# Optimization experiments

Hardware: AMD Instinct MI355X
Metric: run time of the kernel (lower is better)

## Reference

```python
import jax, jax.numpy as jnp
import numpy as np
import math

D_MODEL = 1024
HEADS = 16
HEAD_DIM = D_MODEL // HEADS
BATCH = 2
SEQ = 2048


def setup_inputs() -> dict:
    key = jax.random.key(0)
    ks = jax.random.split(key, 6)
    scale = 1.0 / math.sqrt(D_MODEL)
    return {
        "x": jax.random.normal(ks[0], (BATCH, SEQ, D_MODEL), dtype=jnp.float32),
        "mask": jnp.zeros((SEQ, SEQ), dtype=jnp.float32),
        "w_qkv": jax.random.normal(ks[1], (D_MODEL, 3 * D_MODEL), dtype=jnp.float32) * scale,
        "b_qkv": jax.random.normal(ks[2], (3 * D_MODEL,), dtype=jnp.float32) * 0.01,
        "w_out": jax.random.normal(ks[3], (D_MODEL, D_MODEL), dtype=jnp.float32) * scale,
        "b_out": jax.random.normal(ks[4], (D_MODEL,), dtype=jnp.float32) * 0.01,
    }


def reference(x, mask, w_qkv, b_qkv, w_out, b_out):
    B, S, D = x.shape
    H, hd = HEADS, HEAD_DIM
    # fused QKV projection: [B,S,3D]
    qkv = x @ w_qkv + b_qkv
    # [B,S,H,3*hd] -> [B,H,S,3*hd]
    qkv = qkv.reshape(B, S, H, 3 * hd).transpose(0, 2, 1, 3)
    q, k, v = jnp.split(qkv, 3, axis=-1)  # each [B,H,S,hd]
    inv_sqrt_d = jnp.asarray(1.0 / math.sqrt(hd), dtype=x.dtype)
    scores = jnp.einsum("bhqd,bhkd->bhqk", q, k) * inv_sqrt_d
    # additive mask; [S,S] broadcasts identically in [H,B,S,S] or [B,H,S,S] layout
    scores = scores + mask
    attn = jax.nn.softmax(scores, axis=-1)
    vals = jnp.einsum("bhqk,bhkd->bhqd", attn, v)  # [B,H,S,hd]
    vals = vals.transpose(0, 2, 1, 3).reshape(B, S, H * hd)
    return vals @ w_out + b_out
```

## Files before the change

### kernel.cpp

```cpp
#include <hip/hip_runtime.h>


typedef __bf16 bf16;
typedef __bf16 bf16x2 __attribute__((ext_vector_type(2)));
typedef __bf16 bf16x4 __attribute__((ext_vector_type(4)));
typedef __bf16 bf16x8 __attribute__((ext_vector_type(8)));
typedef float f32x4 __attribute__((ext_vector_type(4)));

#define MFMA(a, b, c) __builtin_amdgcn_mfma_f32_16x16x32_bf16((a), (b), (c), 0, 0, 0)

#if __has_builtin(__builtin_amdgcn_exp2f)
#define EXP2(x) __builtin_amdgcn_exp2f(x)
#else
#define EXP2(x) exp2f(x)
#endif

__device__ __forceinline__ void load_lds16(const bf16* g, void* l) {
    __builtin_amdgcn_global_load_lds(
        (const __attribute__((address_space(1))) unsigned int*)g,
        (__attribute__((address_space(3))) unsigned int*)l, 16, 0, 0);
}

__global__ void cast4_kernel(const float* __restrict__ in, bf16* __restrict__ out, int n4) {
    int i = blockIdx.x * blockDim.x + threadIdx.x;
    if (i < n4) {
        float4 v = ((const float4*)in)[i];
        bf16x4 o = {(bf16)v.x, (bf16)v.y, (bf16)v.z, (bf16)v.w};
        ((bf16x4*)out)[i] = o;
    }
}

__global__ void transpose_cast_kernel(const float* __restrict__ in, bf16* __restrict__ out,
                                      int R, int C) {
    __shared__ float tile[32][33];
    int bx = blockIdx.x * 32;
    int by = blockIdx.y * 32;
    int tx = threadIdx.x, ty = threadIdx.y;
    for (int i = 0; i < 32; i += 8)
        tile[ty + i][tx] = in[(size_t)(by + ty + i) * C + bx + tx];
    __syncthreads();
    for (int i = 0; i < 32; i += 8)
        out[(size_t)(bx + ty + i) * R + by + tx] = (bf16)tile[tx][ty + i];
}

__global__ __launch_bounds__(256) void gemm_qkv_kernel(
    const bf16* __restrict__ A, const bf16* __restrict__ BT,
    const float* __restrict__ bias,
    bf16* __restrict__ Q, bf16* __restrict__ K, bf16* __restrict__ VT) {
    __shared__ __attribute__((aligned(16))) char lds[2][16384];
    int bm = blockIdx.x, bn = blockIdx.y;
    int t = threadIdx.x;
    int w = t >> 6, lane = t & 63, g = lane >> 4, l16 = lane & 15;
    int wm = (w >> 1) * 64, wn = (w & 1) * 64;
    f32x4 acc[4][4] = {};
    const bf16* Ablk = A + (size_t)(bm * 128) * 1024;
    const bf16* Bblk = BT + (size_t)(bn * 128) * 1024;
    int srow = t >> 2;
    int scg = (t & 3) ^ (srow & 3);
    const bf16* ag0 = Ablk + (size_t)srow * 1024 + scg * 8;
    const bf16* ag1 = ag0 + 64 * 1024;
    const bf16* bg0 = Bblk + (size_t)srow * 1024 + scg * 8;
    const bf16* bg1 = bg0 + 64 * 1024;

    load_lds16(ag0, lds[0] + t * 16);
    load_lds16(ag1, lds[0] + 4096 + t * 16);
    load_lds16(bg0, lds[0] + 8192 + t * 16);
    load_lds16(bg1, lds[0] + 12288 + t * 16);
    asm volatile("s_waitcnt vmcnt(0)" ::: "memory");

    int sw = l16 & 3;
#pragma unroll 2
    for (int j = 0; j < 32; j++) {
        asm volatile("s_barrier" ::: "memory");
        int jp = j + 1 < 32 ? j + 1 : 31;
        char* dst = lds[(j + 1) & 1];
        load_lds16(ag0 + jp * 32, dst + t * 16);
        load_lds16(ag1 + jp * 32, dst + 4096 + t * 16);
        load_lds16(bg0 + jp * 32, dst + 8192 + t * 16);
        load_lds16(bg1 + jp * 32, dst + 12288 + t * 16);

        const bf16* As = (const bf16*)lds[j & 1];
        const bf16* Bs = (const bf16*)(lds[j & 1] + 8192);
        bf16x8 af[4], bfr[4];
#pragma unroll
        for (int mi = 0; mi < 4; mi++) {
            int row = wm + mi * 16 + l16;
            af[mi] = *(const bf16x8*)(&As[row * 32 + (g ^ sw) * 8]);
        }
#pragma unroll
        for (int ni = 0; ni < 4; ni++) {
            int row = wn + ni * 16 + l16;
            bfr[ni] = *(const bf16x8*)(&Bs[row * 32 + (g ^ sw) * 8]);
        }
#pragma unroll
        for (int mi = 0; mi < 4; mi++)
#pragma unroll
            for (int ni = 0; ni < 4; ni++)
                acc[mi][ni] = MFMA(bfr[ni], af[mi], acc[mi][ni]);
        asm volatile("s_waitcnt vmcnt(0)" ::: "memory");
    }
    __syncthreads();

    bf16* vt = (bf16*)lds;
    int b = bm >> 4;
    int row0 = (bm & 15) * 128 + wm;
    int half_col = bn * 128 + wn;
    int h = half_col / 192, tt = half_col % 192;
    size_t bh = (size_t)(b * 16 + h);

    if (tt < 128) {
        bf16* base = (tt == 0 ? Q : K) + bh * 2048 * 64;
#pragma unroll
        for (int mi = 0; mi < 4; mi++) {
#pragma unroll
            for (int ni = 0; ni < 4; ni++) {
                int d0 = ni * 16 + g * 4;
                float4 bv = *(const float4*)(&bias[half_col + d0]);
                int s = row0 + mi * 16 + l16;
                bf16x4 pk = {(bf16)(acc[mi][ni][0] + bv.x), (bf16)(acc[mi][ni][1] + bv.y),
                             (bf16)(acc[mi][ni][2] + bv.z), (bf16)(acc[mi][ni][3] + bv.w)};
                *(bf16x4*)(&base[(size_t)s * 64 + d0]) = pk;
            }
        }
    } else {
#pragma unroll
        for (int mi = 0; mi < 4; mi++) {
            int s_local = wm + mi * 16 + l16;
#pragma unroll
            for (int ni = 0; ni < 4; ni++) {
                int d0 = ni * 16 + g * 4;
                float4 bv = *(const float4*)(&bias[half_col + d0]);
                vt[(d0 + 0) * 136 + s_local] = (bf16)(acc[mi][ni][0] + bv.x);
                vt[(d0 + 1) * 136 + s_local] = (bf16)(acc[mi][ni][1] + bv.y);
                vt[(d0 + 2) * 136 + s_local] = (bf16)(acc[mi][ni][2] + bv.z);
                vt[(d0 + 3) * 136 + s_local] = (bf16)(acc[mi][ni][3] + bv.w);
            }
        }
    }
    __syncthreads();

    int hc0 = bn * 128, hc1 = bn * 128 + 64;
    int vhalf = (hc0 % 192 == 128) ? 0 : ((hc1 % 192 == 128) ? 1 : -1);
    if (vhalf >= 0) {
        int vcol = bn * 128 + vhalf * 64;
        size_t vbh = (size_t)(b * 16 + vcol / 192);
        int d = t >> 2, ch = t & 3;
        const bf16* src = &vt[d * 136 + ch * 32];
        bf16* dstp = &VT[(vbh * 64 + d) * 2048 + (bm & 15) * 128 + ch * 32];
#pragma unroll
        for (int k = 0; k < 4; k++)
            *(bf16x8*)(&dstp[k * 8]) = *(const bf16x8*)(&src[k * 8]);
    }
}

__global__ __launch_bounds__(256) void gemm_out_kernel(
    const bf16* __restrict__ A, const bf16* __restrict__ BT,
    const float* __restrict__ bias, float* __restrict__ out) {
    __shared__ __attribute__((aligned(16))) char lds[2][12288];
    int bm = blockIdx.x, bn = blockIdx.y;
    int t = threadIdx.x;
    int w = t >> 6, lane = t & 63, g = lane >> 4, l16 = lane & 15;
    int wm = (w >> 1) * 64, wn = (w & 1) * 32;
    f32x4 acc[4][2] = {};
    const bf16* Ablk = A + (size_t)(bm * 128) * 1024;
    const bf16* Bblk = BT + (size_t)(bn * 64) * 1024;
    int srow = t >> 2;
    int scg = (t & 3) ^ (srow & 3);
    const bf16* ag0 = Ablk + (size_t)srow * 1024 + scg * 8;
    const bf16* ag1 = ag0 + 64 * 1024;
    const bf16* bg0 = Bblk + (size_t)srow * 1024 + scg * 8;

    load_lds16(ag0, lds[0] + t * 16);
    load_lds16(ag1, lds[0] + 4096 + t * 16);
    load_lds16(bg0, lds[0] + 8192 + t * 16);
    asm volatile("s_waitcnt vmcnt(0)" ::: "memory");

    int sw = l16 & 3;
#pragma unroll 2
    for (int j = 0; j < 32; j++) {
        asm volatile("s_barrier" ::: "memory");
        int jp = j + 1 < 32 ? j + 1 : 31;
        char* dst = lds[(j + 1) & 1];
        load_lds16(ag0 + jp * 32, dst + t * 16);
        load_lds16(ag1 + jp * 32, dst + 4096 + t * 16);
        load_lds16(bg0 + jp * 32, dst + 8192 + t * 16);

        const bf16* As = (const bf16*)lds[j & 1];
        const bf16* Bs = (const bf16*)(lds[j & 1] + 8192);
        bf16x8 af[4], bfr[2];
#pragma unroll
        for (int mi = 0; mi < 4; mi++) {
            int row = wm + mi * 16 + l16;
            af[mi] = *(const bf16x8*)(&As[row * 32 + (g ^ sw) * 8]);
        }
#pragma unroll
        for (int ni = 0; ni < 2; ni++) {
            int row = wn + ni * 16 + l16;
            bfr[ni] = *(const bf16x8*)(&Bs[row * 32 + (g ^ sw) * 8]);
        }
#pragma unroll
        for (int mi = 0; mi < 4; mi++)
#pragma unroll
            for (int ni = 0; ni < 2; ni++)
                acc[mi][ni] = MFMA(bfr[ni], af[mi], acc[mi][ni]);
        asm volatile("s_waitcnt vmcnt(0)" ::: "memory");
    }

#pragma unroll
    for (int mi = 0; mi < 4; mi++) {
#pragma unroll
        for (int ni = 0; ni < 2; ni++) {
            int row = bm * 128 + wm + mi * 16 + l16;
            int col0 = bn * 64 + wn + ni * 16 + g * 4;
            float4 bv = *(const float4*)(&bias[col0]);
            float4 ov = {acc[mi][ni][0] + bv.x, acc[mi][ni][1] + bv.y,
                         acc[mi][ni][2] + bv.z, acc[mi][ni][3] + bv.w};
            *(float4*)(&out[(size_t)row * 1024 + col0]) = ov;
        }
    }
}

__global__ __launch_bounds__(256, 2) void attn_kernel(
    const bf16* __restrict__ Q, const bf16* __restrict__ K,
    const bf16* __restrict__ VT, const float* __restrict__ mask,
    bf16* __restrict__ vals) {
    __shared__ __attribute__((aligned(16))) char lds[4][8192];

    int blk = blockIdx.x;
    int bh = ((blk & 7) << 2) | ((blk >> 3) & 3);
    int qt = blk >> 5;
    int t = threadIdx.x;
    int w = t >> 6, lane = t & 63, g = lane >> 4, l16 = lane & 15;
    int qw = qt * 128 + w * 32;

    const bf16* Qp = Q + (size_t)bh * 2048 * 64;
    const bf16* Kp = K + (size_t)bh * 2048 * 64;
    const bf16* Vp = VT + (size_t)bh * 64 * 2048;
    const float* mrowA = mask + (size_t)(qw + l16) * 2048;
    const float* mrowB = mask + (size_t)(qw + 16 + l16) * 2048;

    int ks_row = t >> 3;
    int ks_cblk = (t & 7) ^ (ks_row & 7);
    const bf16* kg = Kp + ks_row * 64 + ks_cblk * 8;
    int vs_d = t >> 2;
    int vs_sblk = (t & 3) ^ ((t >> 3) & 3);
    const bf16* vg = Vp + (size_t)vs_d * 2048 + vs_sblk * 8;

    const float SCL = 0.125f * 1.44269504089f;
    const float L2E = 1.44269504089f;

    bf16x8 qa0 = *(const bf16x8*)(&Qp[(size_t)(qw + l16) * 64 + g * 8]);
    bf16x8 qa1 = *(const bf16x8*)(&Qp[(size_t)(qw + l16) * 64 + 32 + g * 8]);
    bf16x8 qb0 = *(const bf16x8*)(&Qp[(size_t)(qw + 16 + l16) * 64 + g * 8]);
    bf16x8 qb1 = *(const bf16x8*)(&Qp[(size_t)(qw + 16 + l16) * 64 + 32 + g * 8]);
    load_lds16(kg + 0, &lds[0][t * 16]);
    load_lds16(vg + 0, &lds[0][4096 + t * 16]);
    float4 mva0 = *(const float4*)(&mrowA[0 + g * 4]);
    float4 mva1 = *(const float4*)(&mrowA[16 + g * 4]);
    float4 mvb0 = *(const float4*)(&mrowB[0 + g * 4]);
    float4 mvb1 = *(const float4*)(&mrowB[16 + g * 4]);
    load_lds16(kg + 1 * 32 * 64, &lds[1][t * 16]);
    load_lds16(vg + 1 * 32, &lds[1][4096 + t * 16]);
    asm volatile("s_waitcnt vmcnt(0)" ::: "memory");
    asm volatile("s_barrier" ::: "memory");

    f32x4 o[4][2] = {};
    float la = 0.f, lb = 0.f;

    for (int j = 0; j < 64; j++) {
        int buf = j & 3;
        int jm = j + 1 < 64 ? j + 1 : 63;
        float4 nmva0 = *(const float4*)(&mrowA[jm * 32 + g * 4]);
        float4 nmva1 = *(const float4*)(&mrowA[jm * 32 + 16 + g * 4]);
        float4 nmvb0 = *(const float4*)(&mrowB[jm * 32 + g * 4]);
        float4 nmvb1 = *(const float4*)(&mrowB[jm * 32 + 16 + g * 4]);
        int jp = j + 2 < 64 ? j + 2 : 63;
        load_lds16(kg + (size_t)jp * 32 * 64, &lds[(j + 2) & 3][t * 16]);
        load_lds16(vg + jp * 32, &lds[(j + 2) & 3][4096 + t * 16]);
        asm volatile("s_waitcnt vmcnt(12)" ::: "memory");
        asm volatile("s_barrier" ::: "memory");

        float pa[8], pb[8];
#pragma unroll
        for (int ts = 0; ts < 2; ts++) {
            int s0 = ts * 16 + l16;
            int swz = s0 & 7;
            bf16x8 k0 = *(const bf16x8*)(&lds[buf][(s0 * 8 + (g ^ swz)) * 16]);
            bf16x8 k1 = *(const bf16x8*)(&lds[buf][(s0 * 8 + ((4 + g) ^ swz)) * 16]);
            f32x4 sta = {}, stb = {};
            sta = MFMA(k0, qa0, sta);
            sta = MFMA(k1, qa1, sta);
            stb = MFMA(k0, qb0, stb);
            stb = MFMA(k1, qb1, stb);
            float4 ma = ts ? mva1 : mva0;
            float4 mb = ts ? mvb1 : mvb0;
            pa[ts * 4 + 0] = EXP2(sta[0] * SCL + ma.x * L2E);
            pa[ts * 4 + 1] = EXP2(sta[1] * SCL + ma.y * L2E);
            pa[ts * 4 + 2] = EXP2(sta[2] * SCL + ma.z * L2E);
            pa[ts * 4 + 3] = EXP2(sta[3] * SCL + ma.w * L2E);
            pb[ts * 4 + 0] = EXP2(stb[0] * SCL + mb.x * L2E);
            pb[ts * 4 + 1] = EXP2(stb[1] * SCL + mb.y * L2E);
            pb[ts * 4 + 2] = EXP2(stb[2] * SCL + mb.z * L2E);
            pb[ts * 4 + 3] = EXP2(stb[3] * SCL + mb.w * L2E);
        }
#pragma unroll
        for (int i = 0; i < 8; i++) { la += pa[i]; lb += pb[i]; }

        int selA = (((2 * g) & 3) << 4) | l16;
        int selB = (((2 * g + 1) & 3) << 4) | l16;
        bool hi = (g & 2) != 0;
        union { int i[4]; bf16x8 v; } pua, pub;
        {
            union { bf16x2 h; int i; } u;
            int dw0, dw1, dw2, dw3;
            u.h = bf16x2{(bf16)pa[0], (bf16)pa[1]}; dw0 = u.i;
            u.h = bf16x2{(bf16)pa[2], (bf16)pa[3]}; dw1 = u.i;
            u.h = bf16x2{(bf16)pa[4], (bf16)pa[5]}; dw2 = u.i;
            u.h = bf16x2{(bf16)pa[6], (bf16)pa[7]}; dw3 = u.i;
            int t0a = __shfl(dw0, selA, 64), t2a = __shfl(dw2, selA, 64);
            int t1a = __shfl(dw1, selA, 64), t3a = __shfl(dw3, selA, 64);
            int t0b = __shfl(dw0, selB, 64), t2b = __shfl(dw2, selB, 64);
            int t1b = __shfl(dw1, selB, 64), t3b = __shfl(dw3, selB, 64);
            pua.i[0] = hi ? t2a : t0a;
            pua.i[1] = hi ? t3a : t1a;
            pua.i[2] = hi ? t2b : t0b;
            pua.i[3] = hi ? t3b : t1b;
        }
        {
            union { bf16x2 h; int i; } u;
            int dw0, dw1, dw2, dw3;
            u.h = bf16x2{(bf16)pb[0], (bf16)pb[1]}; dw0 = u.i;
            u.h = bf16x2{(bf16)pb[2], (bf16)pb[3]}; dw1 = u.i;
            u.h = bf16x2{(bf16)pb[4], (bf16)pb[5]}; dw2 = u.i;
            u.h = bf16x2{(bf16)pb[6], (bf16)pb[7]}; dw3 = u.i;
            int t0a = __shfl(dw0, selA, 64), t2a = __shfl(dw2, selA, 64);
            int t1a = __shfl(dw1, selA, 64), t3a = __shfl(dw3, selA, 64);
            int t0b = __shfl(dw0, selB, 64), t2b = __shfl(dw2, selB, 64);
            int t1b = __shfl(dw1, selB, 64), t3b = __shfl(dw3, selB, 64);
            pub.i[0] = hi ? t2a : t0a;
            pub.i[1] = hi ? t3a : t1a;
            pub.i[2] = hi ? t2b : t0b;
            pub.i[3] = hi ? t3b : t1b;
        }

#pragma unroll
        for (int nc = 0; nc < 4; nc++) {
            int d = nc * 16 + l16;
            int slot = d * 4 + (g ^ ((d >> 1) & 3));
            bf16x8 vf = *(const bf16x8*)(&lds[buf][4096 + slot * 16]);
            o[nc][0] = MFMA(vf, pua.v, o[nc][0]);
            o[nc][1] = MFMA(vf, pub.v, o[nc][1]);
        }

        mva0 = nmva0; mva1 = nmva1;
        mvb0 = nmvb0; mvb1 = nmvb1;
    }
    asm volatile("s_waitcnt vmcnt(0)" ::: "memory");

    la += __shfl_xor(la, 16, 64);
    la += __shfl_xor(la, 32, 64);
    lb += __shfl_xor(lb, 16, 64);
    lb += __shfl_xor(lb, 32, 64);
    int b = bh >> 4, h = bh & 15;
    float lia = 1.f / la, lib = 1.f / lb;
    size_t rowA = (size_t)(b * 2048 + qw + l16);
    size_t rowB = rowA + 16;
#pragma unroll
    for (int nc = 0; nc < 4; nc++) {
        bf16x4 pkA = {(bf16)(o[nc][0][0] * lia), (bf16)(o[nc][0][1] * lia),
                      (bf16)(o[nc][0][2] * lia), (bf16)(o[nc][0][3] * lia)};
        *(bf16x4*)(&vals[rowA * 1024 + h * 64 + nc * 16 + g * 4]) = pkA;
        bf16x4 pkB = {(bf16)(o[nc][1][0] * lib), (bf16)(o[nc][1][1] * lib),
                      (bf16)(o[nc][1][2] * lib), (bf16)(o[nc][1][3] * lib)};
        *(bf16x4*)(&vals[rowB * 1024 + h * 64 + nc * 16 + g * 4]) = pkB;
    }
}

extern "C" void kernel_launch(void* const* d_in, const int* in_sizes, int n_in,
                              void* d_out, int out_size, void* d_ws, size_t ws_size,
                              hipStream_t stream) {
    const float* x     = (const float*)d_in[0];
    const float* mask  = (const float*)d_in[1];
    const float* w_qkv = (const float*)d_in[2];
    const float* b_qkv = (const float*)d_in[3];
    const float* w_out = (const float*)d_in[4];
    const float* b_out = (const float*)d_in[5];
    float* out = (float*)d_out;

    char* ws = (char*)d_ws;
    size_t off = 0;
    bf16* xb    = (bf16*)(ws + off); off += (size_t)4096 * 1024 * 2;
    bf16* wqkvT = (bf16*)(ws + off); off += (size_t)3072 * 1024 * 2;
    bf16* woutT = (bf16*)(ws + off); off += (size_t)1024 * 1024 * 2;
    bf16* Qa    = (bf16*)(ws + off); off += (size_t)32 * 2048 * 64 * 2;
    bf16* Ka    = (bf16*)(ws + off); off += (size_t)32 * 2048 * 64 * 2;
    bf16* VTa   = (bf16*)(ws + off); off += (size_t)32 * 64 * 2048 * 2;
    bf16* vals  = (bf16*)(ws + off); off += (size_t)4096 * 1024 * 2;

    cast4_kernel<<<4096, 256, 0, stream>>>(x, xb, 4096 * 1024 / 4);
    transpose_cast_kernel<<<dim3(96, 32), dim3(32, 8), 0, stream>>>(w_qkv, wqkvT, 1024, 3072);
    transpose_cast_kernel<<<dim3(32, 32), dim3(32, 8), 0, stream>>>(w_out, woutT, 1024, 1024);
    gemm_qkv_kernel<<<dim3(32, 24), 256, 0, stream>>>(xb, wqkvT, b_qkv, Qa, Ka, VTa);
    attn_kernel<<<512, 256, 0, stream>>>(Qa, Ka, VTa, mask, vals);
    gemm_out_kernel<<<dim3(32, 16), 256, 0, stream>>>(vals, woutT, b_out, out);
}
```

Measured before the change: 230.7 us.

## Split attention key range across two warp groups and merge partials via LDS

Each attention block now has 512 threads, i.e. two groups of four warps over the same query tile. Each group processes half of the key sequence with its own LDS pipeline slice. Because the kernel's softmax uses no running max, the partial outputs and row sums can be merged by plain addition through LDS before the final normalized write. The goal is more waves per CU and a shorter per-block loop to hide latency. The risk is register pressure from the tighter launch bounds (possible spills), plus the extra LDS use and barriers.

Result: slower. 257.5 us (+11.6%).

```diff
diff --git a/kernel.cpp b/kernel.cpp
--- a/kernel.cpp
+++ b/kernel.cpp
@@ -220,31 +220,36 @@
     }
 }
 
-__global__ __launch_bounds__(256, 2) void attn_kernel(
+__global__ __launch_bounds__(512, 4) void attn_kernel(
     const bf16* __restrict__ Q, const bf16* __restrict__ K,
     const bf16* __restrict__ VT, const float* __restrict__ mask,
     bf16* __restrict__ vals) {
-    __shared__ __attribute__((aligned(16))) char lds[4][8192];
+    __shared__ __attribute__((aligned(16))) char lds[4][16384];
 
     int blk = blockIdx.x;
     int bh = ((blk & 7) << 2) | ((blk >> 3) & 3);
     int qt = blk >> 5;
     int t = threadIdx.x;
     int w = t >> 6, lane = t & 63, g = lane >> 4, l16 = lane & 15;
-    int qw = qt * 128 + w * 32;
+    int wq = w & 3;
+    int c = w >> 2;
+    int tl = t & 255;
+    int qw = qt * 128 + wq * 32;
+    int koff = c << 10;
 
     const bf16* Qp = Q + (size_t)bh * 2048 * 64;
     const bf16* Kp = K + (size_t)bh * 2048 * 64;
     const bf16* Vp = VT + (size_t)bh * 64 * 2048;
-    const float* mrowA = mask + (size_t)(qw + l16) * 2048;
-    const float* mrowB = mask + (size_t)(qw + 16 + l16) * 2048;
-
-    int ks_row = t >> 3;
-    int ks_cblk = (t & 7) ^ (ks_row & 7);
-    const bf16* kg = Kp + ks_row * 64 + ks_cblk * 8;
-    int vs_d = t >> 2;
-    int vs_sblk = (t & 3) ^ ((t >> 3) & 3);
-    const bf16* vg = Vp + (size_t)vs_d * 2048 + vs_sblk * 8;
+    const float* mrowA = mask + (size_t)(qw + l16) * 2048 + koff;
+    const float* mrowB = mask + (size_t)(qw + 16 + l16) * 2048 + koff;
+
+    int ks_row = tl >> 3;
+    int ks_cblk = (tl & 7) ^ (ks_row & 7);
+    const bf16* kg = Kp + (size_t)(koff + ks_row) * 64 + ks_cblk * 8;
+    int vs_d = tl >> 2;
+    int vs_sblk = (tl & 3) ^ ((tl >> 3) & 3);
+    const bf16* vg = Vp + (size_t)vs_d * 2048 + koff + vs_sblk * 8;
+    char* ldsc = lds[0] + c * 8192;
 
     const float SCL = 0.125f * 1.44269504089f;
     const float L2E = 1.44269504089f;
@@ -253,30 +258,31 @@
     bf16x8 qa1 = *(const bf16x8*)(&Qp[(size_t)(qw + l16) * 64 + 32 + g * 8]);
     bf16x8 qb0 = *(const bf16x8*)(&Qp[(size_t)(qw + 16 + l16) * 64 + g * 8]);
     bf16x8 qb1 = *(const bf16x8*)(&Qp[(size_t)(qw + 16 + l16) * 64 + 32 + g * 8]);
-    load_lds16(kg + 0, &lds[0][t * 16]);
-    load_lds16(vg + 0, &lds[0][4096 + t * 16]);
+    load_lds16(kg + 0, ldsc + tl * 16);
+    load_lds16(vg + 0, ldsc + 4096 + tl * 16);
     float4 mva0 = *(const float4*)(&mrowA[0 + g * 4]);
     float4 mva1 = *(const float4*)(&mrowA[16 + g * 4]);
     float4 mvb0 = *(const float4*)(&mrowB[0 + g * 4]);
     float4 mvb1 = *(const float4*)(&mrowB[16 + g * 4]);
-    load_lds16(kg + 1 * 32 * 64, &lds[1][t * 16]);
-    load_lds16(vg + 1 * 32, &lds[1][4096 + t * 16]);
+    load_lds16(kg + 1 * 32 * 64, ldsc + 16384 + tl * 16);
+    load_lds16(vg + 1 * 32, ldsc + 16384 + 4096 + tl * 16);
     asm volatile("s_waitcnt vmcnt(0)" ::: "memory");
     asm volatile("s_barrier" ::: "memory");
 
     f32x4 o[4][2] = {};
     float la = 0.f, lb = 0.f;
 
-    for (int j = 0; j < 64; j++) {
-        int buf = j & 3;
-        int jm = j + 1 < 64 ? j + 1 : 63;
+    for (int j = 0; j < 32; j++) {
+        const char* bufp = lds[j & 3] + c * 8192;
+        int jm = j + 1 < 32 ? j + 1 : 31;
         float4 nmva0 = *(const float4*)(&mrowA[jm * 32 + g * 4]);
         float4 nmva1 = *(const float4*)(&mrowA[jm * 32 + 16 + g * 4]);
         float4 nmvb0 = *(const float4*)(&mrowB[jm * 32 + g * 4]);
         float4 nmvb1 = *(const float4*)(&mrowB[jm * 32 + 16 + g * 4]);
-        int jp = j + 2 < 64 ? j + 2 : 63;
-        load_lds16(kg + (size_t)jp * 32 * 64, &lds[(j + 2) & 3][t * 16]);
-        load_lds16(vg + jp * 32, &lds[(j + 2) & 3][4096 + t * 16]);
+        int jp = j + 2 < 32 ? j + 2 : 31;
+        char* dstp = lds[(j + 2) & 3] + c * 8192;
+        load_lds16(kg + (size_t)jp * 32 * 64, dstp + tl * 16);
+        load_lds16(vg + jp * 32, dstp + 4096 + tl * 16);
         asm volatile("s_waitcnt vmcnt(12)" ::: "memory");
         asm volatile("s_barrier" ::: "memory");
 
@@ -285,8 +291,8 @@
         for (int ts = 0; ts < 2; ts++) {
             int s0 = ts * 16 + l16;
             int swz = s0 & 7;
-            bf16x8 k0 = *(const bf16x8*)(&lds[buf][(s0 * 8 + (g ^ swz)) * 16]);
-            bf16x8 k1 = *(const bf16x8*)(&lds[buf][(s0 * 8 + ((4 + g) ^ swz)) * 16]);
+            bf16x8 k0 = *(const bf16x8*)(&bufp[(s0 * 8 + (g ^ swz)) * 16]);
+            bf16x8 k1 = *(const bf16x8*)(&bufp[(s0 * 8 + ((4 + g) ^ swz)) * 16]);
             f32x4 sta = {}, stb = {};
             sta = MFMA(k0, qa0, sta);
             sta = MFMA(k1, qa1, sta);
@@ -347,7 +353,7 @@
         for (int nc = 0; nc < 4; nc++) {
             int d = nc * 16 + l16;
             int slot = d * 4 + (g ^ ((d >> 1) & 3));
-            bf16x8 vf = *(const bf16x8*)(&lds[buf][4096 + slot * 16]);
+            bf16x8 vf = *(const bf16x8*)(&bufp[4096 + slot * 16]);
             o[nc][0] = MFMA(vf, pua.v, o[nc][0]);
             o[nc][1] = MFMA(vf, pub.v, o[nc][1]);
         }
@@ -361,18 +367,42 @@
     la += __shfl_xor(la, 32, 64);
     lb += __shfl_xor(lb, 16, 64);
     lb += __shfl_xor(lb, 32, 64);
-    int b = bh >> 4, h = bh & 15;
-    float lia = 1.f / la, lib = 1.f / lb;
-    size_t rowA = (size_t)(b * 2048 + qw + l16);
-    size_t rowB = rowA + 16;
-#pragma unroll
-    for (int nc = 0; nc < 4; nc++) {
-        bf16x4 pkA = {(bf16)(o[nc][0][0] * lia), (bf16)(o[nc][0][1] * lia),
-                      (bf16)(o[nc][0][2] * lia), (bf16)(o[nc][0][3] * lia)};
-        *(bf16x4*)(&vals[rowA * 1024 + h * 64 + nc * 16 + g * 4]) = pkA;
-        bf16x4 pkB = {(bf16)(o[nc][1][0] * lib), (bf16)(o[nc][1][1] * lib),
-                      (bf16)(o[nc][1][2] * lib), (bf16)(o[nc][1][3] * lib)};
-        *(bf16x4*)(&vals[rowB * 1024 + h * 64 + nc * 16 + g * 4]) = pkB;
+
+    __syncthreads();
+    float* xch = (float*)lds;
+    float* po = xch + wq * 2304;
+    if (c == 1) {
+#pragma unroll
+        for (int nc = 0; nc < 4; nc++)
+#pragma unroll
+            for (int gp = 0; gp < 2; gp++)
+                *(f32x4*)(&po[((nc * 2 + gp) * 64 + lane) * 4]) = o[nc][gp];
+        po[2048 + lane] = la;
+        po[2048 + 64 + lane] = lb;
+    }
+    __syncthreads();
+    if (c == 0) {
+#pragma unroll
+        for (int nc = 0; nc < 4; nc++)
+#pragma unroll
+            for (int gp = 0; gp < 2; gp++)
+                o[nc][gp] += *(const f32x4*)(&po[((nc * 2 + gp) * 64 + lane) * 4]);
+        la += po[2048 + lane];
+        lb += po[2048 + 64 + lane];
+
+        int b = bh >> 4, h = bh & 15;
+        float lia = 1.f / la, lib = 1.f / lb;
+        size_t rowA = (size_t)(b * 2048 + qw + l16);
+        size_t rowB = rowA + 16;
+#pragma unroll
+        for (int nc = 0; nc < 4; nc++) {
+            bf16x4 pkA = {(bf16)(o[nc][0][0] * lia), (bf16)(o[nc][0][1] * lia),
+                          (bf16)(o[nc][0][2] * lia), (bf16)(o[nc][0][3] * lia)};
+            *(bf16x4*)(&vals[rowA * 1024 + h * 64 + nc * 16 + g * 4]) = pkA;
+            bf16x4 pkB = {(bf16)(o[nc][1][0] * lib), (bf16)(o[nc][1][1] * lib),
+                          (bf16)(o[nc][1][2] * lib), (bf16)(o[nc][1][3] * lib)};
+            *(bf16x4*)(&vals[rowB * 1024 + h * 64 + nc * 16 + g * 4]) = pkB;
+        }
     }
 }
 
@@ -401,6 +431,6 @@
     transpose_cast_kernel<<<dim3(96, 32), dim3(32, 8), 0, stream>>>(w_qkv, wqkvT, 1024, 3072);
     transpose_cast_kernel<<<dim3(32, 32), dim3(32, 8), 0, stream>>>(w_out, woutT, 1024, 1024);
     gemm_qkv_kernel<<<dim3(32, 24), 256, 0, stream>>>(xb, wqkvT, b_qkv, Qa, Ka, VTa);
-    attn_kernel<<<512, 256, 0, stream>>>(Qa, Ka, VTa, mask, vals);
+    attn_kernel<<<512, 512, 0, stream>>>(Qa, Ka, VTa, mask, vals);
     gemm_out_kernel<<<dim3(32, 16), 256, 0, stream>>>(vals, woutT, b_out, out);
 }
```

## Switch attention inner loop to 32x32x16 MFMA tiles

Applied to the files above, without the earlier changes.

Rewrites the attention kernel's QK^T and PV products to use 32x32x16 bf16 MFMA instructions instead of 16x16x32. Each lane now owns one query row, which simplifies the softmax sum reduction and cuts the P-fragment reshuffle to a single xor-32 swap. The LDS read patterns and the mask loads are remapped to match. The intent is fewer instructions, fewer cross-lane shuffles and fewer LDS reads per tile, at the cost of 16-wide accumulators that raise register pressure.

After: 225.3 us. 1.02x faster.

```diff
diff --git a/kernel.cpp b/kernel.cpp
--- a/kernel.cpp
+++ b/kernel.cpp
@@ -6,8 +6,10 @@
 typedef __bf16 bf16x4 __attribute__((ext_vector_type(4)));
 typedef __bf16 bf16x8 __attribute__((ext_vector_type(8)));
 typedef float f32x4 __attribute__((ext_vector_type(4)));
+typedef float f32x16 __attribute__((ext_vector_type(16)));
 
 #define MFMA(a, b, c) __builtin_amdgcn_mfma_f32_16x16x32_bf16((a), (b), (c), 0, 0, 0)
+#define MFMA32(a, b, c) __builtin_amdgcn_mfma_f32_32x32x16_bf16((a), (b), (c), 0, 0, 0)
 
 #if __has_builtin(__builtin_amdgcn_exp2f)
 #define EXP2(x) __builtin_amdgcn_exp2f(x)
@@ -230,14 +232,14 @@
     int bh = ((blk & 7) << 2) | ((blk >> 3) & 3);
     int qt = blk >> 5;
     int t = threadIdx.x;
-    int w = t >> 6, lane = t & 63, g = lane >> 4, l16 = lane & 15;
+    int w = t >> 6, lane = t & 63;
+    int l32 = lane & 31, hi = lane >> 5;
     int qw = qt * 128 + w * 32;
 
     const bf16* Qp = Q + (size_t)bh * 2048 * 64;
     const bf16* Kp = K + (size_t)bh * 2048 * 64;
     const bf16* Vp = VT + (size_t)bh * 64 * 2048;
-    const float* mrowA = mask + (size_t)(qw + l16) * 2048;
-    const float* mrowB = mask + (size_t)(qw + 16 + l16) * 2048;
+    const float* mrow = mask + (size_t)(qw + l32) * 2048;
 
     int ks_row = t >> 3;
     int ks_cblk = (t & 7) ^ (ks_row & 7);
@@ -249,130 +251,144 @@
     const float SCL = 0.125f * 1.44269504089f;
     const float L2E = 1.44269504089f;
 
-    bf16x8 qa0 = *(const bf16x8*)(&Qp[(size_t)(qw + l16) * 64 + g * 8]);
-    bf16x8 qa1 = *(const bf16x8*)(&Qp[(size_t)(qw + l16) * 64 + 32 + g * 8]);
-    bf16x8 qb0 = *(const bf16x8*)(&Qp[(size_t)(qw + 16 + l16) * 64 + g * 8]);
-    bf16x8 qb1 = *(const bf16x8*)(&Qp[(size_t)(qw + 16 + l16) * 64 + 32 + g * 8]);
-    load_lds16(kg + 0, &lds[0][t * 16]);
-    load_lds16(vg + 0, &lds[0][4096 + t * 16]);
-    float4 mva0 = *(const float4*)(&mrowA[0 + g * 4]);
-    float4 mva1 = *(const float4*)(&mrowA[16 + g * 4]);
-    float4 mvb0 = *(const float4*)(&mrowB[0 + g * 4]);
-    float4 mvb1 = *(const float4*)(&mrowB[16 + g * 4]);
-    load_lds16(kg + 1 * 32 * 64, &lds[1][t * 16]);
-    load_lds16(vg + 1 * 32, &lds[1][4096 + t * 16]);
+    bf16x8 qf[4];
+#pragma unroll
+    for (int t4 = 0; t4 < 4; t4++)
+        qf[t4] = *(const bf16x8*)(&Qp[(size_t)(qw + l32) * 64 + t4 * 16 + hi * 8]);
+
+    load_lds16(kg + 0, lds[0] + t * 16);
+    load_lds16(vg + 0, lds[0] + 4096 + t * 16);
+    float4 mc0 = *(const float4*)(&mrow[0 + hi * 4]);
+    float4 mc1 = *(const float4*)(&mrow[8 + hi * 4]);
+    float4 mc2 = *(const float4*)(&mrow[16 + hi * 4]);
+    float4 mc3 = *(const float4*)(&mrow[24 + hi * 4]);
+    load_lds16(kg + 32 * 64, lds[1] + t * 16);
+    load_lds16(vg + 32, lds[1] + 4096 + t * 16);
     asm volatile("s_waitcnt vmcnt(0)" ::: "memory");
     asm volatile("s_barrier" ::: "memory");
 
-    f32x4 o[4][2] = {};
-    float la = 0.f, lb = 0.f;
+    f32x16 o0 = {}, o1 = {};
+    const f32x16 kZero = {};
+    float la = 0.f;
 
     for (int j = 0; j < 64; j++) {
-        int buf = j & 3;
+        const char* bufp = lds[j & 3];
         int jm = j + 1 < 64 ? j + 1 : 63;
-        float4 nmva0 = *(const float4*)(&mrowA[jm * 32 + g * 4]);
-        float4 nmva1 = *(const float4*)(&mrowA[jm * 32 + 16 + g * 4]);
-        float4 nmvb0 = *(const float4*)(&mrowB[jm * 32 + g * 4]);
-        float4 nmvb1 = *(const float4*)(&mrowB[jm * 32 + 16 + g * 4]);
+        float4 nm0 = *(const float4*)(&mrow[jm * 32 + 0 + hi * 4]);
+        float4 nm1 = *(const float4*)(&mrow[jm * 32 + 8 + hi * 4]);
+        float4 nm2 = *(const float4*)(&mrow[jm * 32 + 16 + hi * 4]);
+        float4 nm3 = *(const float4*)(&mrow[jm * 32 + 24 + hi * 4]);
         int jp = j + 2 < 64 ? j + 2 : 63;
-        load_lds16(kg + (size_t)jp * 32 * 64, &lds[(j + 2) & 3][t * 16]);
-        load_lds16(vg + jp * 32, &lds[(j + 2) & 3][4096 + t * 16]);
+        char* dstp = lds[(j + 2) & 3];
+        load_lds16(kg + (size_t)jp * 32 * 64, dstp + t * 16);
+        load_lds16(vg + jp * 32, dstp + 4096 + t * 16);
         asm volatile("s_waitcnt vmcnt(12)" ::: "memory");
         asm volatile("s_barrier" ::: "memory");
 
-        float pa[8], pb[8];
-#pragma unroll
-        for (int ts = 0; ts < 2; ts++) {
-            int s0 = ts * 16 + l16;
-            int swz = s0 & 7;
-            bf16x8 k0 = *(const bf16x8*)(&lds[buf][(s0 * 8 + (g ^ swz)) * 16]);
-            bf16x8 k1 = *(const bf16x8*)(&lds[buf][(s0 * 8 + ((4 + g) ^ swz)) * 16]);
-            f32x4 sta = {}, stb = {};
-            sta = MFMA(k0, qa0, sta);
-            sta = MFMA(k1, qa1, sta);
-            stb = MFMA(k0, qb0, stb);
-            stb = MFMA(k1, qb1, stb);
-            float4 ma = ts ? mva1 : mva0;
-            float4 mb = ts ? mvb1 : mvb0;
-            pa[ts * 4 + 0] = EXP2(sta[0] * SCL + ma.x * L2E);
-            pa[ts * 4 + 1] = EXP2(sta[1] * SCL + ma.y * L2E);
-            pa[ts * 4 + 2] = EXP2(sta[2] * SCL + ma.z * L2E);
-            pa[ts * 4 + 3] = EXP2(sta[3] * SCL + ma.w * L2E);
-            pb[ts * 4 + 0] = EXP2(stb[0] * SCL + mb.x * L2E);
-            pb[ts * 4 + 1] = EXP2(stb[1] * SCL + mb.y * L2E);
-            pb[ts * 4 + 2] = EXP2(stb[2] * SCL + mb.z * L2E);
-            pb[ts * 4 + 3] = EXP2(stb[3] * SCL + mb.w * L2E);
-        }
-#pragma unroll
-        for (int i = 0; i < 8; i++) { la += pa[i]; lb += pb[i]; }
-
-        int selA = (((2 * g) & 3) << 4) | l16;
-        int selB = (((2 * g + 1) & 3) << 4) | l16;
-        bool hi = (g & 2) != 0;
-        union { int i[4]; bf16x8 v; } pua, pub;
+        f32x16 s;
         {
-            union { bf16x2 h; int i; } u;
-            int dw0, dw1, dw2, dw3;
-            u.h = bf16x2{(bf16)pa[0], (bf16)pa[1]}; dw0 = u.i;
-            u.h = bf16x2{(bf16)pa[2], (bf16)pa[3]}; dw1 = u.i;
-            u.h = bf16x2{(bf16)pa[4], (bf16)pa[5]}; dw2 = u.i;
-            u.h = bf16x2{(bf16)pa[6], (bf16)pa[7]}; dw3 = u.i;
-            int t0a = __shfl(dw0, selA, 64), t2a = __shfl(dw2, selA, 64);
-            int t1a = __shfl(dw1, selA, 64), t3a = __shfl(dw3, selA, 64);
-            int t0b = __shfl(dw0, selB, 64), t2b = __shfl(dw2, selB, 64);
-            int t1b = __shfl(dw1, selB, 64), t3b = __shfl(dw3, selB, 64);
-            pua.i[0] = hi ? t2a : t0a;
-            pua.i[1] = hi ? t3a : t1a;
-            pua.i[2] = hi ? t2b : t0b;
-            pua.i[3] = hi ? t3b : t1b;
-        }
+            int slot0 = l32 * 8 + ((2 * 0 + hi) ^ (l32 & 7));
+            bf16x8 kf0 = *(const bf16x8*)(&bufp[slot0 * 16]);
+            s = MFMA32(kf0, qf[0], kZero);
+            int slot1 = l32 * 8 + ((2 * 1 + hi) ^ (l32 & 7));
+            bf16x8 kf1 = *(const bf16x8*)(&bufp[slot1 * 16]);
+            s = MFMA32(kf1, qf[1], s);
+            int slot2 = l32 * 8 + ((2 * 2 + hi) ^ (l32 & 7));
+            bf16x8 kf2 = *(const bf16x8*)(&bufp[slot2 * 16]);
+            s = MFMA32(kf2, qf[2], s);
+            int slot3 = l32 * 8 + ((2 * 3 + hi) ^ (l32 & 7));
+            bf16x8 kf3 = *(const bf16x8*)(&bufp[slot3 * 16]);
+            s = MFMA32(kf3, qf[3], s);
+        }
+
+        float p[16];
+        p[0]  = EXP2(s[0] * SCL + mc0.x * L2E);
+        p[1]  = EXP2(s[1] * SCL + mc0.y * L2E);
+        p[2]  = EXP2(s[2] * SCL + mc0.z * L2E);
+        p[3]  = EXP2(s[3] * SCL + mc0.w * L2E);
+        p[4]  = EXP2(s[4] * SCL + mc1.x * L2E);
+        p[5]  = EXP2(s[5] * SCL + mc1.y * L2E);
+        p[6]  = EXP2(s[6] * SCL + mc1.z * L2E);
+        p[7]  = EXP2(s[7] * SCL + mc1.w * L2E);
+        p[8]  = EXP2(s[8] * SCL + mc2.x * L2E);
+        p[9]  = EXP2(s[9] * SCL + mc2.y * L2E);
+        p[10] = EXP2(s[10] * SCL + mc2.z * L2E);
+        p[11] = EXP2(s[11] * SCL + mc2.w * L2E);
+        p[12] = EXP2(s[12] * SCL + mc3.x * L2E);
+        p[13] = EXP2(s[13] * SCL + mc3.y * L2E);
+        p[14] = EXP2(s[14] * SCL + mc3.z * L2E);
+        p[15] = EXP2(s[15] * SCL + mc3.w * L2E);
         {
-            union { bf16x2 h; int i; } u;
-            int dw0, dw1, dw2, dw3;
-            u.h = bf16x2{(bf16)pb[0], (bf16)pb[1]}; dw0 = u.i;
-            u.h = bf16x2{(bf16)pb[2], (bf16)pb[3]}; dw1 = u.i;
-            u.h = bf16x2{(bf16)pb[4], (bf16)pb[5]}; dw2 = u.i;
-            u.h = bf16x2{(bf16)pb[6], (bf16)pb[7]}; dw3 = u.i;
-            int t0a = __shfl(dw0, selA, 64), t2a = __shfl(dw2, selA, 64);
-            int t1a = __shfl(dw1, selA, 64), t3a = __shfl(dw3, selA, 64);
-            int t0b = __shfl(dw0, selB, 64), t2b = __shfl(dw2, selB, 64);
-            int t1b = __shfl(dw1, selB, 64), t3b = __shfl(dw3, selB, 64);
-            pub.i[0] = hi ? t2a : t0a;
-            pub.i[1] = hi ? t3a : t1a;
-            pub.i[2] = hi ? t2b : t0b;
-            pub.i[3] = hi ? t3b : t1b;
-        }
-
-#pragma unroll
-        for (int nc = 0; nc < 4; nc++) {
-            int d = nc * 16 + l16;
-            int slot = d * 4 + (g ^ ((d >> 1) & 3));
-            bf16x8 vf = *(const bf16x8*)(&lds[buf][4096 + slot * 16]);
-            o[nc][0] = MFMA(vf, pua.v, o[nc][0]);
-            o[nc][1] = MFMA(vf, pub.v, o[nc][1]);
-        }
-
-        mva0 = nmva0; mva1 = nmva1;
-        mvb0 = nmvb0; mvb1 = nmvb1;
+            float a0 = p[0] + p[1], a1 = p[2] + p[3], a2 = p[4] + p[5], a3 = p[6] + p[7];
+            float a4 = p[8] + p[9], a5 = p[10] + p[11], a6 = p[12] + p[13], a7 = p[14] + p[15];
+            float b0 = a0 + a1, b1 = a2 + a3, b2 = a4 + a5, b3 = a6 + a7;
+            la += (b0 + b1) + (b2 + b3);
+        }
+
+        unsigned dw0, dw1, dw2, dw3, dw4, dw5, dw6, dw7;
+        {
+            union { bf16x2 h; unsigned u; } u;
+            u.h = bf16x2{(bf16)p[0],  (bf16)p[1]};  dw0 = u.u;
+            u.h = bf16x2{(bf16)p[2],  (bf16)p[3]};  dw1 = u.u;
+            u.h = bf16x2{(bf16)p[4],  (bf16)p[5]};  dw2 = u.u;
+            u.h = bf16x2{(bf16)p[6],  (bf16)p[7]};  dw3 = u.u;
+            u.h = bf16x2{(bf16)p[8],  (bf16)p[9]};  dw4 = u.u;
+            u.h = bf16x2{(bf16)p[10], (bf16)p[11]}; dw5 = u.u;
+            u.h = bf16x2{(bf16)p[12], (bf16)p[13]}; dw6 = u.u;
+            u.h = bf16x2{(bf16)p[14], (bf16)p[15]}; dw7 = u.u;
+        }
+        int sx0 = __shfl_xor((int)dw0, 32, 64);
+        int sx1 = __shfl_xor((int)dw1, 32, 64);
+        int sx2 = __shfl_xor((int)dw2, 32, 64);
+        int sx3 = __shfl_xor((int)dw3, 32, 64);
+        int sx4 = __shfl_xor((int)dw4, 32, 64);
+        int sx5 = __shfl_xor((int)dw5, 32, 64);
+        int sx6 = __shfl_xor((int)dw6, 32, 64);
+        int sx7 = __shfl_xor((int)dw7, 32, 64);
+        bool hib = hi != 0;
+        union { unsigned u[4]; bf16x8 v; } pb0, pb1;
+        pb0.u[0] = hib ? (unsigned)sx2 : dw0;
+        pb0.u[1] = hib ? (unsigned)sx3 : dw1;
+        pb0.u[2] = hib ? dw2 : (unsigned)sx0;
+        pb0.u[3] = hib ? dw3 : (unsigned)sx1;
+        pb1.u[0] = hib ? (unsigned)sx6 : dw4;
+        pb1.u[1] = hib ? (unsigned)sx7 : dw5;
+        pb1.u[2] = hib ? dw6 : (unsigned)sx4;
+        pb1.u[3] = hib ? dw7 : (unsigned)sx5;
+
+        {
+            int d0 = l32;
+            int d1 = 32 + l32;
+            int sv00 = d0 * 4 + ((2 * 0 + hi) ^ ((d0 >> 1) & 3));
+            int sv01 = d0 * 4 + ((2 * 1 + hi) ^ ((d0 >> 1) & 3));
+            int sv10 = d1 * 4 + ((2 * 0 + hi) ^ ((d1 >> 1) & 3));
+            int sv11 = d1 * 4 + ((2 * 1 + hi) ^ ((d1 >> 1) & 3));
+            bf16x8 vf00 = *(const bf16x8*)(&bufp[4096 + sv00 * 16]);
+            bf16x8 vf01 = *(const bf16x8*)(&bufp[4096 + sv01 * 16]);
+            bf16x8 vf10 = *(const bf16x8*)(&bufp[4096 + sv10 * 16]);
+            bf16x8 vf11 = *(const bf16x8*)(&bufp[4096 + sv11 * 16]);
+            o0 = MFMA32(vf00, pb0.v, o0);
+            o0 = MFMA32(vf01, pb1.v, o0);
+            o1 = MFMA32(vf10, pb0.v, o1);
+            o1 = MFMA32(vf11, pb1.v, o1);
+        }
+
+        mc0 = nm0; mc1 = nm1; mc2 = nm2; mc3 = nm3;
     }
     asm volatile("s_waitcnt vmcnt(0)" ::: "memory");
 
-    la += __shfl_xor(la, 16, 64);
     la += __shfl_xor(la, 32, 64);
-    lb += __shfl_xor(lb, 16, 64);
-    lb += __shfl_xor(lb, 32, 64);
-    int b = bh >> 4, h = bh & 15;
-    float lia = 1.f / la, lib = 1.f / lb;
-    size_t rowA = (size_t)(b * 2048 + qw + l16);
-    size_t rowB = rowA + 16;
-#pragma unroll
-    for (int nc = 0; nc < 4; nc++) {
-        bf16x4 pkA = {(bf16)(o[nc][0][0] * lia), (bf16)(o[nc][0][1] * lia),
-                      (bf16)(o[nc][0][2] * lia), (bf16)(o[nc][0][3] * lia)};
-        *(bf16x4*)(&vals[rowA * 1024 + h * 64 + nc * 16 + g * 4]) = pkA;
-        bf16x4 pkB = {(bf16)(o[nc][1][0] * lib), (bf16)(o[nc][1][1] * lib),
-                      (bf16)(o[nc][1][2] * lib), (bf16)(o[nc][1][3] * lib)};
-        *(bf16x4*)(&vals[rowB * 1024 + h * 64 + nc * 16 + g * 4]) = pkB;
+    int b = bh >> 4, hh = bh & 15;
+    float li = 1.f / la;
+    size_t row = (size_t)(b * 2048 + qw + l32);
+#pragma unroll
+    for (int rg = 0; rg < 4; rg++) {
+        bf16x4 pk0 = {(bf16)(o0[rg * 4 + 0] * li), (bf16)(o0[rg * 4 + 1] * li),
+                      (bf16)(o0[rg * 4 + 2] * li), (bf16)(o0[rg * 4 + 3] * li)};
+        *(bf16x4*)(&vals[row * 1024 + hh * 64 + rg * 8 + hi * 4]) = pk0;
+        bf16x4 pk1 = {(bf16)(o1[rg * 4 + 0] * li), (bf16)(o1[rg * 4 + 1] * li),
+                      (bf16)(o1[rg * 4 + 2] * li), (bf16)(o1[rg * 4 + 3] * li)};
+        *(bf16x4*)(&vals[row * 1024 + hh * 64 + 32 + rg * 8 + hi * 4]) = pk1;
     }
 }
 
```
